# Kernel optimization log

Hardware: AMD Instinct MI355X
Metric: run time of the kernel (lower is better)

Reference implementation:

```python
import jax, jax.numpy as jnp
import numpy as np

N = 8192
SPIKE_THRESHOLD = 30.0
PRE_SPIKE_SENSITIVITY = 4.0
TAU_G = 6.5
W_MEAN, W_VAR = 0.2, 0.3


def setup_inputs() -> dict:
    key = jax.random.key(0)
    ks = jax.random.split(key, 6)
    c0, d0 = -65.0, 8.0
    return {
        "x_in": jax.random.normal(ks[0], (N,), jnp.float32),
        "v": c0 + jax.random.normal(ks[1], (N,), jnp.float32),
        "u": d0 + jax.random.normal(ks[2], (N,), jnp.float32),
        "g": jax.random.uniform(ks[3], (N,), jnp.float32),
        "w": W_MEAN - W_VAR + 2.0 * W_VAR * jax.random.uniform(ks[4], (N, N), jnp.float32),
        "a_p": jnp.full((N,), 0.02, jnp.float32),
        "b_p": jnp.full((N,), 0.25, jnp.float32),
        "c_p": jnp.full((N,), c0, jnp.float32),
        "d_p": jnp.full((N,), d0, jnp.float32),
    }


def reference(x_in, v, u, g, w, a_p, b_p, c_p, d_p):
    # synaptic input: [N,N] @ [N] + [N]
    I = w @ g + x_in
    # membrane potential update (Izhikevich quadratic dynamics)
    v1 = v + (0.04 * v * v + 5.0 * v + 140.0 - u + I)
    # differentiable spike surrogate (returned)
    spiked_s = jax.nn.sigmoid(PRE_SPIKE_SENSITIVITY * (v1 - SPIKE_THRESHOLD))
    # hard spike mask for state resets
    spiked = (v1 >= SPIKE_THRESHOLD).astype(v1.dtype)
    not_spiked = 1.0 - spiked
    dg = -g / TAU_G
    du = jnp.abs(a_p) * (jnp.abs(b_p) * v1 - u)
    v_out = not_spiked * v1 + spiked * c_p
    u_out = not_spiked * (u + du) + spiked * d_p
    g_out = not_spiked * (g + dg) + spiked  # spiked * 1.0
    # module returns (self.v, self.spiked); u_out/g_out are hidden state
    return v_out, spiked_s, u_out, g_out
```

## Files before the change

### kernel.cpp

```cpp
#include <hip/hip_runtime.h>
#include <cmath>


#define NN 8192
#define WAVES_PER_BLOCK 4
#define BLOCK (WAVES_PER_BLOCK * 64)

__global__ __launch_bounds__(BLOCK) void izh_kernel(
    const float* __restrict__ x_in,
    const float* __restrict__ v,
    const float* __restrict__ u,
    const float* __restrict__ g,
    const float* __restrict__ w,
    const float* __restrict__ a_p,
    const float* __restrict__ b_p,
    const float* __restrict__ c_p,
    const float* __restrict__ d_p,
    float* __restrict__ out)
{
    __shared__ float4 g_lds[NN / 4];

    const int tid = threadIdx.x;

    const float4* g4 = (const float4*)g;
    #pragma unroll
    for (int i = 0; i < (NN / 4) / BLOCK; ++i) {
        g_lds[tid + i * BLOCK] = g4[tid + i * BLOCK];
    }
    __syncthreads();

    const int wave = tid >> 6;
    const int lane = tid & 63;
    const int row  = blockIdx.x * WAVES_PER_BLOCK + wave;

    const float4* w4 = (const float4*)(w + (size_t)row * NN);
    float acc0 = 0.0f, acc1 = 0.0f, acc2 = 0.0f, acc3 = 0.0f;
    #pragma unroll 8
    for (int k = 0; k < 32; ++k) {
        const int idx = lane + 64 * k;
        float4 wv = w4[idx];
        float4 gv = g_lds[idx];
        acc0 = fmaf(wv.x, gv.x, acc0);
        acc1 = fmaf(wv.y, gv.y, acc1);
        acc2 = fmaf(wv.z, gv.z, acc2);
        acc3 = fmaf(wv.w, gv.w, acc3);
    }
    float acc = (acc0 + acc1) + (acc2 + acc3);

    #pragma unroll
    for (int off = 32; off > 0; off >>= 1) {
        acc += __shfl_down(acc, off, 64);
    }

    if (lane == 0) {
        const float I  = acc + x_in[row];
        const float vv = v[row];
        const float uu = u[row];
        const float gg = g[row];

        const float v1 = vv + (0.04f * vv * vv + 5.0f * vv + 140.0f - uu + I);

        const float s = 1.0f / (1.0f + expf(-4.0f * (v1 - 30.0f)));

        const float spiked = (v1 >= 30.0f) ? 1.0f : 0.0f;
        const float ns     = 1.0f - spiked;

        const float du = fabsf(a_p[row]) * (fabsf(b_p[row]) * v1 - uu);
        const float dg = -gg / 6.5f;

        out[0 * NN + row] = ns * v1 + spiked * c_p[row];
        out[1 * NN + row] = s;
        out[2 * NN + row] = ns * (uu + du) + spiked * d_p[row];
        out[3 * NN + row] = ns * (gg + dg) + spiked;
    }
}

extern "C" void kernel_launch(void* const* d_in, const int* in_sizes, int n_in,
                              void* d_out, int out_size, void* d_ws, size_t ws_size,
                              hipStream_t stream) {
    const float* x_in = (const float*)d_in[0];
    const float* v    = (const float*)d_in[1];
    const float* u    = (const float*)d_in[2];
    const float* g    = (const float*)d_in[3];
    const float* w    = (const float*)d_in[4];
    const float* a_p  = (const float*)d_in[5];
    const float* b_p  = (const float*)d_in[6];
    const float* c_p  = (const float*)d_in[7];
    const float* d_p  = (const float*)d_in[8];
    float* out = (float*)d_out;

    const int grid = NN / WAVES_PER_BLOCK;
    izh_kernel<<<grid, BLOCK, 0, stream>>>(x_in, v, u, g, w, a_p, b_p, c_p, d_p, out);
}
```

Before: 365.3 us.

## Assign one block per row with up-front nontemporal loads of w

Changes the work split from one wave per row to one 256-thread block per row, so the grid grows to 8192 blocks. Each thread issues all eight of its w vector loads at once as nontemporal loads before the multiply-accumulate. Per-wave partial sums are combined through shared memory. The aim is more memory-level parallelism on the w stream, but each block now stages the whole g vector into LDS, which quadruples that traffic and adds an extra barrier.

Measured after the change: 349.3 us. -4.4%, faster.

```diff
diff --git a/kernel.cpp b/kernel.cpp
--- a/kernel.cpp
+++ b/kernel.cpp
@@ -3,8 +3,9 @@
 
 
 #define NN 8192
-#define WAVES_PER_BLOCK 4
-#define BLOCK (WAVES_PER_BLOCK * 64)
+#define BLOCK 256
+
+typedef float f4 __attribute__((ext_vector_type(4)));
 
 __global__ __launch_bounds__(BLOCK) void izh_kernel(
     const float* __restrict__ x_in,
@@ -18,32 +19,36 @@
     const float* __restrict__ d_p,
     float* __restrict__ out)
 {
-    __shared__ float4 g_lds[NN / 4];
+    __shared__ f4 g_lds[NN / 4];
+    __shared__ float wave_part[BLOCK / 64];
 
-    const int tid = threadIdx.x;
+    const int tid  = threadIdx.x;
+    const int row  = blockIdx.x;
+    const int lane = tid & 63;
+    const int wave = tid >> 6;
 
-    const float4* g4 = (const float4*)g;
+    const f4* g4 = (const f4*)g;
     #pragma unroll
     for (int i = 0; i < (NN / 4) / BLOCK; ++i) {
         g_lds[tid + i * BLOCK] = g4[tid + i * BLOCK];
     }
     __syncthreads();
 
-    const int wave = tid >> 6;
-    const int lane = tid & 63;
-    const int row  = blockIdx.x * WAVES_PER_BLOCK + wave;
+    const f4* w4 = (const f4*)(w + (size_t)row * NN);
+    f4 wv[8];
+    #pragma unroll
+    for (int k = 0; k < 8; ++k) {
+        wv[k] = __builtin_nontemporal_load(&w4[tid + BLOCK * k]);
+    }
 
-    const float4* w4 = (const float4*)(w + (size_t)row * NN);
     float acc0 = 0.0f, acc1 = 0.0f, acc2 = 0.0f, acc3 = 0.0f;
-    #pragma unroll 8
-    for (int k = 0; k < 32; ++k) {
-        const int idx = lane + 64 * k;
-        float4 wv = w4[idx];
-        float4 gv = g_lds[idx];
-        acc0 = fmaf(wv.x, gv.x, acc0);
-        acc1 = fmaf(wv.y, gv.y, acc1);
-        acc2 = fmaf(wv.z, gv.z, acc2);
-        acc3 = fmaf(wv.w, gv.w, acc3);
+    #pragma unroll
+    for (int k = 0; k < 8; ++k) {
+        const f4 gv = g_lds[tid + BLOCK * k];
+        acc0 = fmaf(wv[k].x, gv.x, acc0);
+        acc1 = fmaf(wv[k].y, gv.y, acc1);
+        acc2 = fmaf(wv[k].z, gv.z, acc2);
+        acc3 = fmaf(wv[k].w, gv.w, acc3);
     }
     float acc = (acc0 + acc1) + (acc2 + acc3);
 
@@ -51,9 +56,14 @@
     for (int off = 32; off > 0; off >>= 1) {
         acc += __shfl_down(acc, off, 64);
     }
+    if (lane == 0) wave_part[wave] = acc;
+    __syncthreads();
 
-    if (lane == 0) {
-        const float I  = acc + x_in[row];
+    if (tid == 0) {
+        const float dot = (wave_part[0] + wave_part[1])
+                        + (wave_part[2] + wave_part[3]);
+
+        const float I  = dot + x_in[row];
         const float vv = v[row];
         const float uu = u[row];
         const float gg = g[row];
@@ -89,6 +99,5 @@
     const float* d_p  = (const float*)d_in[8];
     float* out = (float*)d_out;
 
-    const int grid = NN / WAVES_PER_BLOCK;
-    izh_kernel<<<grid, BLOCK, 0, stream>>>(x_in, v, u, g, w, a_p, b_p, c_p, d_p, out);
+    izh_kernel<<<NN, BLOCK, 0, stream>>>(x_in, v, u, g, w, a_p, b_p, c_p, d_p, out);
 }
```
